# Kernel optimization log

Hardware: AMD Instinct MI355X
Metric: run time of the kernel (lower is better)

Reference implementation:

```python
import jax, jax.numpy as jnp
import numpy as np

D_MODEL = 1024
NUM_HEADS = 16
D_K = D_MODEL // NUM_HEADS
D_FF = 4096
LN_EPS = 1e-5


def layernorm(x, gamma, beta):
    mu = jnp.mean(x, axis=-1, keepdims=True)
    var = jnp.mean(jnp.square(x - mu), axis=-1, keepdims=True)
    return (x - mu) * jax.lax.rsqrt(var + LN_EPS) * gamma + beta


def setup_inputs() -> dict:
    key = jax.random.key(0)
    ks = jax.random.split(key, 16)
    s = 1.0 / np.sqrt(D_MODEL)
    sf = 1.0 / np.sqrt(D_FF)
    inp = {
        "x": jax.random.normal(ks[0], (2, 2048, D_MODEL), dtype=jnp.float32),
        # attention sublayer LN
        "ln1_g": jnp.ones((D_MODEL,), jnp.float32),
        "ln1_b": jnp.zeros((D_MODEL,), jnp.float32),
        # QKV / output projections, stored as [in, out]
        "Wq": jax.random.uniform(ks[1], (D_MODEL, D_MODEL), jnp.float32, -s, s),
        "bq": jax.random.uniform(ks[2], (D_MODEL,), jnp.float32, -s, s),
        "Wk": jax.random.uniform(ks[3], (D_MODEL, D_MODEL), jnp.float32, -s, s),
        "bk": jax.random.uniform(ks[4], (D_MODEL,), jnp.float32, -s, s),
        "Wv": jax.random.uniform(ks[5], (D_MODEL, D_MODEL), jnp.float32, -s, s),
        "bv": jax.random.uniform(ks[6], (D_MODEL,), jnp.float32, -s, s),
        "Wo": jax.random.uniform(ks[7], (D_MODEL, D_MODEL), jnp.float32, -s, s),
        "bo": jax.random.uniform(ks[8], (D_MODEL,), jnp.float32, -s, s),
        # FFN sublayer LN
        "ln2_g": jnp.ones((D_MODEL,), jnp.float32),
        "ln2_b": jnp.zeros((D_MODEL,), jnp.float32),
        "W1": jax.random.uniform(ks[9], (D_MODEL, D_FF), jnp.float32, -s, s),
        "b1": jax.random.uniform(ks[10], (D_FF,), jnp.float32, -s, s),
        "W2": jax.random.uniform(ks[11], (D_FF, D_MODEL), jnp.float32, -sf, sf),
        "b2": jax.random.uniform(ks[12], (D_MODEL,), jnp.float32, -sf, sf),
    }
    return inp


def block_fwd(x, ln1_g, ln1_b, Wq, bq, Wk, bk, Wv, bv, Wo, bo,
              ln2_g, ln2_b, W1, b1, W2, b2):
    B, S, D = x.shape
    # --- attention sublayer (pre-LN + residual) ---
    h = layernorm(x, ln1_g, ln1_b)
    q = (h @ Wq + bq).reshape(B, S, NUM_HEADS, D_K)
    k = (h @ Wk + bk).reshape(B, S, NUM_HEADS, D_K)
    v = (h @ Wv + bv).reshape(B, S, NUM_HEADS, D_K)
    scale = 1.0 / np.sqrt(D_K)  # == sqrt(d_k)/d_k in source
    attn = jnp.einsum("bqhd,bkhd->bhqk", q, k) * scale  # [B,H,S,S]
    causal = jnp.arange(S)[:, None] >= jnp.arange(S)[None, :]
    attn = jnp.where(causal, attn, -jnp.inf)
    score = jax.nn.softmax(attn, axis=-1)
    o = jnp.einsum("bhqk,bkhd->bqhd", score, v).reshape(B, S, D)
    x = x + (o @ Wo + bo)
    # --- FFN sublayer (pre-LN + residual) ---
    h = layernorm(x, ln2_g, ln2_b)
    h = jax.nn.gelu(h @ W1 + b1, approximate=False)  # torch nn.GELU = exact erf
    return x + (h @ W2 + b2)


def reference(x, ln1_g, ln1_b, Wq, bq, Wk, bk, Wv, bv, Wo, bo,
              ln2_g, ln2_b, W1, b1, W2, b2):
    return block_fwd(x, ln1_g, ln1_b, Wq, bq, Wk, bk, Wv, bv, Wo, bo,
                     ln2_g, ln2_b, W1, b1, W2, b2)
```

## Files before the change

kernel.cpp:

```cpp
#include <hip/hip_runtime.h>
#include <hip/hip_bf16.h>
#include <math.h>

typedef unsigned short u16;
typedef unsigned int u32;
typedef __bf16 bf16x8 __attribute__((ext_vector_type(8)));
typedef float f32x4 __attribute__((ext_vector_type(4)));

#define MFMA16(a, b, c) __builtin_amdgcn_mfma_f32_16x16x32_bf16(a, b, c, 0, 0, 0)

__device__ __forceinline__ u16 f2b(float f) {
    __bf16 h = (__bf16)f;
    return __builtin_bit_cast(u16, h);
}

__device__ __forceinline__ void gld16(const void* g, void* l) {
    __builtin_amdgcn_global_load_lds(
        (const __attribute__((address_space(1))) unsigned int*)g,
        (__attribute__((address_space(3))) unsigned int*)l, 16, 0, 0);
}

__global__ void transpose_convert(const float* __restrict__ in, u16* __restrict__ out,
                                  int R, int C) {
    __shared__ float tile[32][33];
    int c0 = blockIdx.x * 32, r0 = blockIdx.y * 32;
    int tx = threadIdx.x, ty = threadIdx.y;
#pragma unroll
    for (int i = 0; i < 4; i++)
        tile[ty + i * 8][tx] = in[(size_t)(r0 + ty + i * 8) * C + c0 + tx];
    __syncthreads();
#pragma unroll
    for (int i = 0; i < 4; i++)
        out[(size_t)(c0 + ty + i * 8) * R + r0 + tx] = f2b(tile[tx][ty + i * 8]);
}

__global__ __launch_bounds__(256) void ln_kernel(const float* __restrict__ x,
                                                 const float* __restrict__ g,
                                                 const float* __restrict__ b,
                                                 u16* __restrict__ out) {
    int row = blockIdx.x;
    int tid = threadIdx.x;
    const float* xr = x + (size_t)row * 1024;
    float4 v = ((const float4*)xr)[tid];
    float s = v.x + v.y + v.z + v.w;
    float s2 = v.x * v.x + v.y * v.y + v.z * v.z + v.w * v.w;
#pragma unroll
    for (int off = 32; off > 0; off >>= 1) {
        s += __shfl_xor(s, off);
        s2 += __shfl_xor(s2, off);
    }
    __shared__ float ps[4], ps2[4];
    int wid = tid >> 6;
    if ((tid & 63) == 0) { ps[wid] = s; ps2[wid] = s2; }
    __syncthreads();
    s = ps[0] + ps[1] + ps[2] + ps[3];
    s2 = ps2[0] + ps2[1] + ps2[2] + ps2[3];
    float mu = s * (1.0f / 1024.0f);
    float var = s2 * (1.0f / 1024.0f) - mu * mu;
    float rs = rsqrtf(var + 1e-5f);
    int c = tid * 4;
    ushort4 o;
    o.x = f2b((v.x - mu) * rs * g[c + 0] + b[c + 0]);
    o.y = f2b((v.y - mu) * rs * g[c + 1] + b[c + 1]);
    o.z = f2b((v.z - mu) * rs * g[c + 2] + b[c + 2]);
    o.w = f2b((v.w - mu) * rs * g[c + 3] + b[c + 3]);
    ((ushort4*)(out + (size_t)row * 1024))[tid] = o;
}

__global__ __launch_bounds__(256) void vtrans_kernel(const u16* __restrict__ Vb,
                                                     u16* __restrict__ VbT) {
    __shared__ u16 t[64][66];
    const int tid = threadIdx.x;
    const int s0 = blockIdx.x * 64;
    const int bh = blockIdx.y;
    const u16* src = Vb + (size_t)bh * 2048 * 64;
    u16* dst = VbT + (size_t)bh * 64 * 2048;
#pragma unroll
    for (int p = 0; p < 2; p++) {
        int idx = p * 256 + tid;
        int r = idx >> 3, dc = (idx & 7) * 8;
        uint4 v = *(const uint4*)&src[(size_t)(s0 + r) * 64 + dc];
        const u16* pv = (const u16*)&v;
#pragma unroll
        for (int j = 0; j < 8; j++) t[r][dc + j] = pv[j];
    }
    __syncthreads();
    int d = tid >> 2, sc = (tid & 3) * 16;
    u16 buf[16];
#pragma unroll
    for (int m = 0; m < 16; m++) {
        int cp = sc + m;
        int blk = cp >> 5, c = cp & 31;
        int srcw = blk * 32 + (c >> 1) + (c & 1) * 16;
        buf[m] = t[srcw][d];
    }
    *(uint4*)&dst[(size_t)d * 2048 + s0 + sc] = *(uint4*)&buf[0];
    *(uint4*)&dst[(size_t)d * 2048 + s0 + sc + 8] = *(uint4*)&buf[8];
}

#define EPI_QKV 0
#define EPI_RESID 1
#define EPI_GELU 2

__device__ __forceinline__ void gemm_stage(const u16* __restrict__ A,
                                           const u16* __restrict__ BT,
                                           u16 (&Asb)[128][32], u16 (&Bsb)[128][32],
                                           int m0, int n0, int K, int k0, int sr, int sdc,
                                           int wb) {
    gld16(&A[(size_t)(m0 + sr) * K + k0 + sdc], &Asb[0][0] + wb);
    gld16(&A[(size_t)(m0 + 64 + sr) * K + k0 + sdc], &Asb[0][0] + 2048 + wb);
    gld16(&BT[(size_t)(n0 + sr) * K + k0 + sdc], &Bsb[0][0] + wb);
    gld16(&BT[(size_t)(n0 + 64 + sr) * K + k0 + sdc], &Bsb[0][0] + 2048 + wb);
}

__device__ __forceinline__ void gemm_compute(const u16 (&Asb)[128][32],
                                             const u16 (&Bsb)[128][32], f32x4 (&acc)[4][4],
                                             int wm, int wn, int quad, int c15) {
    bf16x8 af[4], bfr[4];
#pragma unroll
    for (int i = 0; i < 4; i++) af[i] = *(const bf16x8*)&Asb[wm + i * 16 + c15][quad * 8];
#pragma unroll
    for (int j = 0; j < 4; j++) bfr[j] = *(const bf16x8*)&Bsb[wn + j * 16 + c15][quad * 8];
#pragma unroll
    for (int i = 0; i < 4; i++)
#pragma unroll
        for (int j = 0; j < 4; j++) acc[i][j] = MFMA16(af[i], bfr[j], acc[i][j]);
}

template <int EPI>
__global__ __launch_bounds__(256) void gemm_kernel(const u16* __restrict__ A,
                                                   const u16* __restrict__ BT,
                                                   const float* __restrict__ bias0,
                                                   const float* __restrict__ bias1,
                                                   const float* __restrict__ bias2,
                                                   void* __restrict__ outp,
                                                   const float* __restrict__ resid,
                                                   int N, int K) {
    __shared__ __align__(16) u16 As0[128][32], Bs0[128][32];
    __shared__ __align__(16) u16 As1[128][32], Bs1[128][32];
    const int tid = threadIdx.x;
    const int m0 = blockIdx.y * 128, n0 = blockIdx.x * 128;
    const int w = tid >> 6, lid = tid & 63, quad = lid >> 4, c15 = lid & 15;
    const int wm = (w >> 1) * 64, wn = (w & 1) * 64;
    const int sr = tid >> 2, sdc = (tid & 3) * 8;
    const int wb = (tid & 192) * 8;

    f32x4 acc[4][4] = {};

    gemm_stage(A, BT, As0, Bs0, m0, n0, K, 0, sr, sdc, wb);
    const int KT = K >> 5;
    for (int kt = 0; kt < KT; kt += 2) {
        __syncthreads();
        gemm_stage(A, BT, As1, Bs1, m0, n0, K, (kt + 1) << 5, sr, sdc, wb);
        gemm_compute(As0, Bs0, acc, wm, wn, quad, c15);
        __syncthreads();
        if (kt + 2 < KT) gemm_stage(A, BT, As0, Bs0, m0, n0, K, (kt + 2) << 5, sr, sdc, wb);
        gemm_compute(As1, Bs1, acc, wm, wn, quad, c15);
    }

    const int which = n0 >> 10;
    const float* bias = (EPI == EPI_QKV) ? (which == 0 ? bias0 : (which == 1 ? bias1 : bias2))
                                         : bias0;
    u16* qkv_dst = (u16*)outp + (size_t)which * 4194304;

#pragma unroll
    for (int i = 0; i < 4; i++) {
#pragma unroll
        for (int j = 0; j < 4; j++) {
#pragma unroll
            for (int r = 0; r < 4; r++) {
                int gr = m0 + wm + i * 16 + quad * 4 + r;
                int gc = n0 + wn + j * 16 + c15;
                if (EPI == EPI_QKV) {
                    int lc = gc & 1023;
                    float v = acc[i][j][r] + bias[lc];
                    int bb = gr >> 11, ss = gr & 2047, hh = lc >> 6, dd = lc & 63;
                    qkv_dst[((size_t)((bb * 16 + hh) * 2048 + ss)) * 64 + dd] = f2b(v);
                } else if (EPI == EPI_RESID) {
                    float v = acc[i][j][r] + bias[gc];
                    ((float*)outp)[(size_t)gr * N + gc] = resid[(size_t)gr * N + gc] + v;
                } else {
                    float v = acc[i][j][r] + bias[gc];
                    float ge = 0.5f * v * (1.0f + erff(v * 0.70710678118654752f));
                    ((u16*)outp)[(size_t)gr * N + gc] = f2b(ge);
                }
            }
        }
    }
}

__device__ __forceinline__ void attn_step(const u16 (&KB)[2][64][32],
                                          const u16 (&VB)[2][64][32],
                                          u16 (&Psw)[2][32][40], const bf16x8 (&aq)[2][2],
                                          f32x4 (&o)[2][4], float (&lsum)[2][4], int kv0,
                                          int qr0, int quad, int c15) {
    if (kv0 > qr0 + 31) return;
    bf16x8 bk[4][2];
#pragma unroll
    for (int nf = 0; nf < 4; nf++)
#pragma unroll
        for (int kd = 0; kd < 2; kd++)
            bk[nf][kd] = *(const bf16x8*)&KB[kd][nf * 16 + c15][quad * 8];
    f32x4 sf[2][4];
#pragma unroll
    for (int qf = 0; qf < 2; qf++)
#pragma unroll
        for (int nf = 0; nf < 4; nf++) {
            f32x4 s = {};
            s = MFMA16(aq[qf][0], bk[nf][0], s);
            s = MFMA16(aq[qf][1], bk[nf][1], s);
            sf[qf][nf] = s;
        }
    const bool domask = (kv0 + 63 > qr0);
    if (domask) {
#pragma unroll
        for (int qf = 0; qf < 2; qf++)
#pragma unroll
            for (int r = 0; r < 4; r++) {
                int rowg = qr0 + qf * 16 + quad * 4 + r;
#pragma unroll
                for (int nf = 0; nf < 4; nf++) {
                    float p = (kv0 + nf * 16 + c15 <= rowg) ? __expf(sf[qf][nf][r] * 0.125f)
                                                            : 0.0f;
                    sf[qf][nf][r] = p;
                    lsum[qf][r] += p;
                }
            }
    } else {
#pragma unroll
        for (int qf = 0; qf < 2; qf++)
#pragma unroll
            for (int r = 0; r < 4; r++)
#pragma unroll
                for (int nf = 0; nf < 4; nf++) {
                    float p = __expf(sf[qf][nf][r] * 0.125f);
                    sf[qf][nf][r] = p;
                    lsum[qf][r] += p;
                }
    }
#pragma unroll
    for (int qf = 0; qf < 2; qf++)
#pragma unroll
        for (int ks = 0; ks < 2; ks++)
#pragma unroll
            for (int r = 0; r < 4; r++) {
                u32 pk = (u32)f2b(sf[qf][2 * ks][r]) | ((u32)f2b(sf[qf][2 * ks + 1][r]) << 16);
                *(u32*)&Psw[ks][qf * 16 + quad * 4 + r][2 * c15] = pk;
            }
    asm volatile("s_waitcnt lgkmcnt(0)" ::: "memory");
    bf16x8 ap[2][2];
#pragma unroll
    for (int qf = 0; qf < 2; qf++)
#pragma unroll
        for (int ks = 0; ks < 2; ks++)
            ap[qf][ks] = *(const bf16x8*)&Psw[ks][qf * 16 + c15][quad * 8];
#pragma unroll
    for (int df = 0; df < 4; df++) {
        bf16x8 bv0 = *(const bf16x8*)&VB[0][df * 16 + c15][quad * 8];
        bf16x8 bv1 = *(const bf16x8*)&VB[1][df * 16 + c15][quad * 8];
#pragma unroll
        for (int qf = 0; qf < 2; qf++) {
            o[qf][df] = MFMA16(ap[qf][0], bv0, o[qf][df]);
            o[qf][df] = MFMA16(ap[qf][1], bv1, o[qf][df]);
        }
    }
}

__global__ __launch_bounds__(256) void attn_kernel(const u16* __restrict__ Q,
                                                   const u16* __restrict__ Kb,
                                                   const u16* __restrict__ VbT,
                                                   u16* __restrict__ attO) {
    __shared__ __align__(16) u16 K0s[2][64][32], K1s[2][64][32];
    __shared__ __align__(16) u16 V0s[2][64][32], V1s[2][64][32];
    __shared__ __align__(16) u16 Ps[4][2][32][40];

    const int tid = threadIdx.x;
    const int bh = blockIdx.x;
    const int pj = blockIdx.y;
    const size_t base = (size_t)bh * 2048 * 64;
    const u16* Qp = Q + base;
    const u16* Kp = Kb + base;
    const u16* Vp = VbT + (size_t)bh * 64 * 2048;
    const int w = tid >> 6, lane = tid & 63, quad = lane >> 4, c15 = lane & 15;
    const int sr = tid >> 2, sdc = (tid & 3) * 8;
    const int wb = (tid & 192) * 8;
    const int bb = bh >> 4, hh = bh & 15;

#define ATTN_STAGE(KB, VB, kvo)                                                        \
    do {                                                                               \
        gld16(&Kp[(size_t)((kvo) + sr) * 64 + sdc], &KB[0][0][0] + wb);                \
        gld16(&Kp[(size_t)((kvo) + sr) * 64 + 32 + sdc], &KB[0][0][0] + 2048 + wb);    \
        gld16(&Vp[(size_t)sr * 2048 + (kvo) + sdc], &VB[0][0][0] + wb);                \
        gld16(&Vp[(size_t)sr * 2048 + (kvo) + 32 + sdc], &VB[0][0][0] + 2048 + wb);    \
    } while (0)

    auto run_tile = [&](int q0) {
        const int qr0 = q0 + w * 32;
        bf16x8 aq[2][2];
#pragma unroll
        for (int qf = 0; qf < 2; qf++)
#pragma unroll
            for (int ks = 0; ks < 2; ks++)
                aq[qf][ks] = *(const bf16x8*)&Qp[(size_t)(qr0 + qf * 16 + c15) * 64 +
                                                 ks * 32 + quad * 8];
        f32x4 o[2][4] = {};
        float lsum[2][4] = {};
        const int steps = (q0 >> 6) + 2;
        __syncthreads();
        ATTN_STAGE(K0s, V0s, 0);
        int s = 0;
        for (;;) {
            __syncthreads();
            if (s + 1 < steps) ATTN_STAGE(K1s, V1s, (s + 1) << 6);
            attn_step(K0s, V0s, Ps[w], aq, o, lsum, s << 6, qr0, quad, c15);
            if (++s >= steps) break;
            __syncthreads();
            if (s + 1 < steps) ATTN_STAGE(K0s, V0s, (s + 1) << 6);
            attn_step(K1s, V1s, Ps[w], aq, o, lsum, s << 6, qr0, quad, c15);
            if (++s >= steps) break;
        }
#pragma unroll
        for (int qf = 0; qf < 2; qf++)
#pragma unroll
            for (int r = 0; r < 4; r++) {
                float l = lsum[qf][r];
#pragma unroll
                for (int off = 1; off < 16; off <<= 1) l += __shfl_xor(l, off);
                float inv = 1.0f / l;
                int sg = qr0 + qf * 16 + quad * 4 + r;
                size_t rowoff = ((size_t)(bb * 2048 + sg)) * 1024 + hh * 64;
#pragma unroll
                for (int df = 0; df < 4; df++)
                    attO[rowoff + df * 16 + c15] = f2b(o[qf][df][r] * inv);
            }
    };
    run_tile((15 - pj) * 128);
    run_tile(pj * 128);
#undef ATTN_STAGE
}

extern "C" void kernel_launch(void* const* d_in, const int* in_sizes, int n_in,
                              void* d_out, int out_size, void* d_ws, size_t ws_size,
                              hipStream_t stream) {
    const float* x = (const float*)d_in[0];
    const float* ln1g = (const float*)d_in[1];
    const float* ln1b = (const float*)d_in[2];
    const float* Wq = (const float*)d_in[3];
    const float* bq = (const float*)d_in[4];
    const float* Wk = (const float*)d_in[5];
    const float* bk = (const float*)d_in[6];
    const float* Wv = (const float*)d_in[7];
    const float* bv = (const float*)d_in[8];
    const float* Wo = (const float*)d_in[9];
    const float* bo = (const float*)d_in[10];
    const float* ln2g = (const float*)d_in[11];
    const float* ln2b = (const float*)d_in[12];
    const float* W1 = (const float*)d_in[13];
    const float* b1 = (const float*)d_in[14];
    const float* W2 = (const float*)d_in[15];
    const float* b2 = (const float*)d_in[16];
    float* out = (float*)d_out;

    char* ws = (char*)d_ws;
    u16* wqkvT = (u16*)(ws + 0);
    u16* woT = (u16*)(ws + 6291456);
    u16* w1T = (u16*)(ws + 8388608);
    u16* w2T = (u16*)(ws + 16777216);
    u16* h = (u16*)(ws + 25165824);
    float* x1 = (float*)(ws + 33554432);
    u16* Qb = (u16*)(ws + 50331648);
    u16* Kb = (u16*)(ws + 58720256);
    u16* Vb = (u16*)(ws + 67108864);
    u16* VbT = (u16*)(ws + 75497472);
    u16* aO = Vb;
    u16* mid = Qb;

    dim3 tb(32, 8);
    transpose_convert<<<dim3(32, 32), tb, 0, stream>>>(Wq, wqkvT, 1024, 1024);
    transpose_convert<<<dim3(32, 32), tb, 0, stream>>>(Wk, wqkvT + 1048576, 1024, 1024);
    transpose_convert<<<dim3(32, 32), tb, 0, stream>>>(Wv, wqkvT + 2097152, 1024, 1024);
    transpose_convert<<<dim3(32, 32), tb, 0, stream>>>(Wo, woT, 1024, 1024);
    transpose_convert<<<dim3(128, 32), tb, 0, stream>>>(W1, w1T, 1024, 4096);
    transpose_convert<<<dim3(32, 128), tb, 0, stream>>>(W2, w2T, 4096, 1024);

    ln_kernel<<<4096, 256, 0, stream>>>(x, ln1g, ln1b, h);

    gemm_kernel<EPI_QKV><<<dim3(24, 32), 256, 0, stream>>>(h, wqkvT, bq, bk, bv, Qb, nullptr,
                                                           3072, 1024);

    vtrans_kernel<<<dim3(32, 32), 256, 0, stream>>>(Vb, VbT);

    attn_kernel<<<dim3(32, 8), 256, 0, stream>>>(Qb, Kb, VbT, aO);

    gemm_kernel<EPI_RESID><<<dim3(8, 32), 256, 0, stream>>>(aO, woT, bo, nullptr, nullptr, x1,
                                                            x, 1024, 1024);

    ln_kernel<<<4096, 256, 0, stream>>>(x1, ln2g, ln2b, h);

    gemm_kernel<EPI_GELU><<<dim3(32, 32), 256, 0, stream>>>(h, w1T, b1, nullptr, nullptr, mid,
                                                            nullptr, 4096, 1024);
    gemm_kernel<EPI_RESID><<<dim3(8, 32), 256, 0, stream>>>(mid, w2T, b2, nullptr, nullptr, out,
                                                            x1, 1024, 4096);
}
```

Baseline: 378.6 us.

## Run FFN down-projection in FP8 with tanh GELU and merged weight transpose

The GELU epilogue now writes its activation as FP8 e4m3 and uses a tanh approximation instead of erf. W2 is transposed into FP8 with a scale of 64, and a new FP8 MFMA GEMM kernel computes the second FFN matmul, dividing the scale back out before bias and residual. The six weight transpose launches are merged into one kernel. This cuts memory traffic and MFMA time for the largest GEMM and removes launch overhead, at the cost of lower numerical precision that may exceed tolerance.

Result: faster. 366.0 us (-3.3%).

```diff
diff --git a/kernel.cpp b/kernel.cpp
--- a/kernel.cpp
+++ b/kernel.cpp
@@ -1,17 +1,26 @@
 #include <hip/hip_runtime.h>
 #include <hip/hip_bf16.h>
+#include <hip/hip_fp8.h>
 #include <math.h>
 
 typedef unsigned short u16;
+typedef unsigned char u8;
 typedef unsigned int u32;
+typedef long i64;
 typedef __bf16 bf16x8 __attribute__((ext_vector_type(8)));
 typedef float f32x4 __attribute__((ext_vector_type(4)));
 
 #define MFMA16(a, b, c) __builtin_amdgcn_mfma_f32_16x16x32_bf16(a, b, c, 0, 0, 0)
+#define MFMA8(a, b, c) __builtin_amdgcn_mfma_f32_16x16x32_fp8_fp8(a, b, c, 0, 0, 0)
 
 __device__ __forceinline__ u16 f2b(float f) {
     __bf16 h = (__bf16)f;
     return __builtin_bit_cast(u16, h);
+}
+
+__device__ __forceinline__ u8 f2f8(float f) {
+    __hip_fp8_e4m3 h(f);
+    return h.__x;
 }
 
 __device__ __forceinline__ void gld16(const void* g, void* l) {
@@ -20,18 +29,46 @@
         (__attribute__((address_space(3))) unsigned int*)l, 16, 0, 0);
 }
 
-__global__ void transpose_convert(const float* __restrict__ in, u16* __restrict__ out,
-                                  int R, int C) {
+__global__ __launch_bounds__(256) void transpose_all(
+    const float* __restrict__ Wq, const float* __restrict__ Wk,
+    const float* __restrict__ Wv, const float* __restrict__ Wo,
+    const float* __restrict__ W1, const float* __restrict__ W2, u16* __restrict__ wqkvT,
+    u16* __restrict__ woT, u16* __restrict__ w1T, u8* __restrict__ w2T8) {
     __shared__ float tile[32][33];
-    int c0 = blockIdx.x * 32, r0 = blockIdx.y * 32;
+    int t = blockIdx.x;
+    const float* in;
+    u16* out = nullptr;
+    int R, C;
+    bool isf8 = false;
+    if (t < 3072) {
+        int m = t >> 10;
+        t &= 1023;
+        in = m == 0 ? Wq : (m == 1 ? Wk : Wv);
+        out = wqkvT + m * 1048576;
+        R = 1024; C = 1024;
+    } else if (t < 4096) {
+        t -= 3072; in = Wo; out = woT; R = 1024; C = 1024;
+    } else if (t < 8192) {
+        t -= 4096; in = W1; out = w1T; R = 1024; C = 4096;
+    } else {
+        t -= 8192; in = W2; R = 4096; C = 1024; isf8 = true;
+    }
+    int tilesX = C >> 5;
+    int c0 = (t % tilesX) * 32, r0 = (t / tilesX) * 32;
     int tx = threadIdx.x, ty = threadIdx.y;
 #pragma unroll
     for (int i = 0; i < 4; i++)
         tile[ty + i * 8][tx] = in[(size_t)(r0 + ty + i * 8) * C + c0 + tx];
     __syncthreads();
-#pragma unroll
-    for (int i = 0; i < 4; i++)
-        out[(size_t)(c0 + ty + i * 8) * R + r0 + tx] = f2b(tile[tx][ty + i * 8]);
+    if (isf8) {
+#pragma unroll
+        for (int i = 0; i < 4; i++)
+            w2T8[(size_t)(c0 + ty + i * 8) * R + r0 + tx] = f2f8(tile[tx][ty + i * 8] * 64.0f);
+    } else {
+#pragma unroll
+        for (int i = 0; i < 4; i++)
+            out[(size_t)(c0 + ty + i * 8) * R + r0 + tx] = f2b(tile[tx][ty + i * 8]);
+    }
 }
 
 __global__ __launch_bounds__(256) void ln_kernel(const float* __restrict__ x,
@@ -181,9 +218,76 @@
                     ((float*)outp)[(size_t)gr * N + gc] = resid[(size_t)gr * N + gc] + v;
                 } else {
                     float v = acc[i][j][r] + bias[gc];
-                    float ge = 0.5f * v * (1.0f + erff(v * 0.70710678118654752f));
-                    ((u16*)outp)[(size_t)gr * N + gc] = f2b(ge);
+                    float u = v * (0.79788456f + 0.03567741f * v * v);
+                    float e = __expf(2.0f * u);
+                    float th = 1.0f - 2.0f / (e + 1.0f);
+                    ((u8*)outp)[(size_t)gr * N + gc] = f2f8(0.5f * v * (1.0f + th));
                 }
+            }
+        }
+    }
+}
+
+__device__ __forceinline__ void gemm8_stage(const u8* __restrict__ A,
+                                            const u8* __restrict__ BT, u8 (&Asb)[128][32],
+                                            u8 (&Bsb)[128][32], int m0, int n0, int K,
+                                            int k0, int sr, int sdc, int wbB) {
+    gld16(&A[(size_t)(m0 + sr) * K + k0 + sdc], &Asb[0][0] + wbB);
+    gld16(&BT[(size_t)(n0 + sr) * K + k0 + sdc], &Bsb[0][0] + wbB);
+}
+
+__device__ __forceinline__ void gemm8_compute(const u8 (&Asb)[128][32],
+                                              const u8 (&Bsb)[128][32], f32x4 (&acc)[4][4],
+                                              int wm, int wn, int quad, int c15) {
+    i64 af[4], bfr[4];
+#pragma unroll
+    for (int i = 0; i < 4; i++) af[i] = *(const i64*)&Asb[wm + i * 16 + c15][quad * 8];
+#pragma unroll
+    for (int j = 0; j < 4; j++) bfr[j] = *(const i64*)&Bsb[wn + j * 16 + c15][quad * 8];
+#pragma unroll
+    for (int i = 0; i < 4; i++)
+#pragma unroll
+        for (int j = 0; j < 4; j++) acc[i][j] = MFMA8(af[i], bfr[j], acc[i][j]);
+}
+
+__global__ __launch_bounds__(256) void gemm_fp8_kernel(const u8* __restrict__ A,
+                                                       const u8* __restrict__ BT,
+                                                       const float* __restrict__ bias,
+                                                       float* __restrict__ outp,
+                                                       const float* __restrict__ resid,
+                                                       int N, int K) {
+    __shared__ __align__(16) u8 As0[128][32], Bs0[128][32];
+    __shared__ __align__(16) u8 As1[128][32], Bs1[128][32];
+    const int tid = threadIdx.x;
+    const int m0 = blockIdx.y * 128, n0 = blockIdx.x * 128;
+    const int w = tid >> 6, lid = tid & 63, quad = lid >> 4, c15 = lid & 15;
+    const int wm = (w >> 1) * 64, wn = (w & 1) * 64;
+    const int sr = tid >> 1, sdc = (tid & 1) * 16;
+    const int wbB = (tid & 192) * 16;
+
+    f32x4 acc[4][4] = {};
+
+    gemm8_stage(A, BT, As0, Bs0, m0, n0, K, 0, sr, sdc, wbB);
+    const int KT = K >> 5;
+    for (int kt = 0; kt < KT; kt += 2) {
+        __syncthreads();
+        gemm8_stage(A, BT, As1, Bs1, m0, n0, K, (kt + 1) << 5, sr, sdc, wbB);
+        gemm8_compute(As0, Bs0, acc, wm, wn, quad, c15);
+        __syncthreads();
+        if (kt + 2 < KT) gemm8_stage(A, BT, As0, Bs0, m0, n0, K, (kt + 2) << 5, sr, sdc, wbB);
+        gemm8_compute(As1, Bs1, acc, wm, wn, quad, c15);
+    }
+
+#pragma unroll
+    for (int i = 0; i < 4; i++) {
+#pragma unroll
+        for (int j = 0; j < 4; j++) {
+#pragma unroll
+            for (int r = 0; r < 4; r++) {
+                int gr = m0 + wm + i * 16 + quad * 4 + r;
+                int gc = n0 + wn + j * 16 + c15;
+                float v = acc[i][j][r] * (1.0f / 64.0f) + bias[gc];
+                outp[(size_t)gr * N + gc] = resid[(size_t)gr * N + gc] + v;
             }
         }
     }
@@ -365,7 +469,7 @@
     u16* wqkvT = (u16*)(ws + 0);
     u16* woT = (u16*)(ws + 6291456);
     u16* w1T = (u16*)(ws + 8388608);
-    u16* w2T = (u16*)(ws + 16777216);
+    u8* w2T8 = (u8*)(ws + 16777216);
     u16* h = (u16*)(ws + 25165824);
     float* x1 = (float*)(ws + 33554432);
     u16* Qb = (u16*)(ws + 50331648);
@@ -373,15 +477,10 @@
     u16* Vb = (u16*)(ws + 67108864);
     u16* VbT = (u16*)(ws + 75497472);
     u16* aO = Vb;
-    u16* mid = Qb;
-
-    dim3 tb(32, 8);
-    transpose_convert<<<dim3(32, 32), tb, 0, stream>>>(Wq, wqkvT, 1024, 1024);
-    transpose_convert<<<dim3(32, 32), tb, 0, stream>>>(Wk, wqkvT + 1048576, 1024, 1024);
-    transpose_convert<<<dim3(32, 32), tb, 0, stream>>>(Wv, wqkvT + 2097152, 1024, 1024);
-    transpose_convert<<<dim3(32, 32), tb, 0, stream>>>(Wo, woT, 1024, 1024);
-    transpose_convert<<<dim3(128, 32), tb, 0, stream>>>(W1, w1T, 1024, 4096);
-    transpose_convert<<<dim3(32, 128), tb, 0, stream>>>(W2, w2T, 4096, 1024);
+    u8* mid8 = (u8*)(ws + 50331648);
+
+    transpose_all<<<12288, dim3(32, 8), 0, stream>>>(Wq, Wk, Wv, Wo, W1, W2, wqkvT, woT,
+                                                     w1T, w2T8);
 
     ln_kernel<<<4096, 256, 0, stream>>>(x, ln1g, ln1b, h);
 
@@ -397,8 +496,7 @@
 
     ln_kernel<<<4096, 256, 0, stream>>>(x1, ln2g, ln2b, h);
 
-    gemm_kernel<EPI_GELU><<<dim3(32, 32), 256, 0, stream>>>(h, w1T, b1, nullptr, nullptr, mid,
+    gemm_kernel<EPI_GELU><<<dim3(32, 32), 256, 0, stream>>>(h, w1T, b1, nullptr, nullptr, mid8,
                                                             nullptr, 4096, 1024);
-    gemm_kernel<EPI_RESID><<<dim3(8, 32), 256, 0, stream>>>(mid, w2T, b2, nullptr, nullptr, out,
-                                                            x1, 1024, 4096);
-}
+    gemm_fp8_kernel<<<dim3(8, 32), 256, 0, stream>>>(mid8, w2T8, b2, out, x1, 1024, 4096);
+}
```
